# Kernel tuning notes

Hardware: AMD Instinct MI355X
Metric: run time of the kernel (lower is better)

Reference implementation:

```python
import jax, jax.numpy as jnp
import numpy as np

B, L, C, D, H = 32, 4096, 64, 512, 720
EPS = 1e-5

def _xavier(key, shape):
    fan_in, fan_out = shape
    lim = float(np.sqrt(6.0 / (fan_in + fan_out)))
    return jax.random.uniform(key, shape, minval=-lim, maxval=lim, dtype=jnp.float32)

def setup_inputs() -> dict:
    key = jax.random.key(0)
    ks = jax.random.split(key, 8)
    return {
        "x": jax.random.normal(ks[0], (B, L, C), dtype=jnp.float32),
        "alpha": jnp.full((C,), 0.5, dtype=jnp.float32),
        "rev_w": jnp.ones((C,), dtype=jnp.float32),
        "rev_b": jnp.zeros((C,), dtype=jnp.float32),
        "se_w": _xavier(ks[1], (C, D)), "se_b": jnp.zeros((D,), jnp.float32),
        "sp_w": _xavier(ks[2], (D, C)), "sp_b": jnp.zeros((C,), jnp.float32),
        "st_w": _xavier(ks[3], (L, H)), "st_b": jnp.zeros((H,), jnp.float32),
        "te_w": _xavier(ks[4], (C, D)), "te_b": jnp.zeros((D,), jnp.float32),
        "tp_w": _xavier(ks[5], (D, C)), "tp_b": jnp.zeros((C,), jnp.float32),
        "tt_w": _xavier(ks[6], (L, H)), "tt_b": jnp.zeros((H,), jnp.float32),
    }

def _path(z, ew, eb, pw, pb, tw, tb):
    # z: (B,L,C) -> embed C->D -> (identity backbone) -> proj D->C -> temporal L->H
    h = z @ ew + eb            # (B,L,D)
    h = h @ pw + pb            # (B,L,C)
    h = jnp.einsum('blc,lh->bhc', h, tw) + tb[None, :, None]  # (B,H,C)
    return h

def reference(x, alpha, rev_w, rev_b, se_w, se_b, sp_w, sp_b, st_w, st_b,
              te_w, te_b, tp_w, tp_b, tt_w, tt_b):
    # RevIN norm (stats detached, var unbiased=False)
    mean = jax.lax.stop_gradient(jnp.mean(x, axis=1, keepdims=True))          # (B,1,C)
    stdev = jax.lax.stop_gradient(jnp.sqrt(jnp.var(x, axis=1, keepdims=True) + EPS))
    xn = (x - mean) / stdev * rev_w + rev_b
    # EMA decomposition: trend[t] = a*trend[t-1] + (1-a)*x[t], trend[0]=x[0]
    a = jax.nn.sigmoid(alpha)  # (C,)
    def step(carry, xt):
        nxt = a * carry + (1.0 - a) * xt
        return nxt, nxt
    t0 = xn[:, 0]                                    # (B,C)
    _, tr = jax.lax.scan(step, t0, jnp.swapaxes(xn, 0, 1)[1:])  # (L-1,B,C)
    trend = jnp.swapaxes(jnp.concatenate([t0[None], tr], axis=0), 0, 1)  # (B,L,C)
    seasonal = xn - trend
    out = _path(seasonal, se_w, se_b, sp_w, sp_b, st_w, st_b) \
        + _path(trend,    te_w, te_b, tp_w, tp_b, tt_w, tt_b)   # (B,H,C)
    # RevIN denorm
    out = (out - rev_b) / (rev_w + EPS)
    out = out * stdev + mean
    return out
```

## Files before the change

kernel.cpp:

```cpp
#include <hip/hip_runtime.h>
#include <hip/hip_bf16.h>
#include <string.h>
#include <stdint.h>

typedef __hip_bfloat16 bf16_t;
typedef float f32x4 __attribute__((ext_vector_type(4)));
typedef short bf16x8 __attribute__((ext_vector_type(8)));

static constexpr int Bn = 32, Ln = 4096, Cn = 64, Hn = 720, HPn = 768;
static constexpr float EPSf = 1e-5f;

static constexpr size_t OSR_SLICE = (size_t)Bn * Hn * Cn;

__device__ __forceinline__ short f2bf(float f) {
  bf16_t h = __float2bfloat16(f);
  unsigned short u; memcpy(&u, &h, 2);
  return (short)u;
}

__device__ __forceinline__ float sigm(float v) { return 1.f / (1.f + expf(-v)); }

__global__ void __launch_bounds__(256) k_prep(const float* __restrict__ se_w, const float* __restrict__ sp_w,
                                              const float* __restrict__ se_b, const float* __restrict__ sp_b,
                                              const float* __restrict__ te_w, const float* __restrict__ tp_w,
                                              const float* __restrict__ te_b, const float* __restrict__ tp_b,
                                              float* __restrict__ M, float* __restrict__ cvec) {
  int p = blockIdx.y, dc = blockIdx.x, t = threadIdx.x;
  const float* ew = p ? te_w : se_w;
  const float* pw = p ? tp_w : sp_w;
  const float* eb = p ? te_b : se_b;
  const float* pb = p ? tp_b : sp_b;
  int d0 = dc * 64;
  __shared__ float ews[64][68];
  __shared__ float pws[64][68];
  __shared__ float ebs[64];
#pragma unroll
  for (int q = 0; q < 4; ++q) {
    int fi = t * 4 + q;
    int r = fi >> 4, dd = (fi * 4) & 63;
    *reinterpret_cast<f32x4*>(&ews[r][dd]) = *reinterpret_cast<const f32x4*>(&ew[r * 512 + d0 + dd]);
    int pdd = fi >> 4, c = (fi * 4) & 63;
    *reinterpret_cast<f32x4*>(&pws[pdd][c]) = *reinterpret_cast<const f32x4*>(&pw[(d0 + pdd) * 64 + c]);
  }
  if (t < 64) ebs[t] = eb[d0 + t];
  __syncthreads();
  int r0 = (t >> 4) * 4, c0 = (t & 15) * 4;
  float acc[4][4];
#pragma unroll
  for (int i = 0; i < 4; ++i)
#pragma unroll
    for (int j = 0; j < 4; ++j) acc[i][j] = 0.f;
#pragma unroll 4
  for (int g = 0; g < 16; ++g) {
    int dd = g * 4;
    f32x4 av[4], bv[4];
#pragma unroll
    for (int i = 0; i < 4; ++i) av[i] = *reinterpret_cast<const f32x4*>(&ews[r0 + i][dd]);
#pragma unroll
    for (int d = 0; d < 4; ++d) bv[d] = *reinterpret_cast<const f32x4*>(&pws[dd + d][c0]);
#pragma unroll
    for (int d = 0; d < 4; ++d)
#pragma unroll
      for (int i = 0; i < 4; ++i)
#pragma unroll
        for (int j = 0; j < 4; ++j) acc[i][j] = fmaf(av[i][d], bv[d][j], acc[i][j]);
  }
#pragma unroll
  for (int i = 0; i < 4; ++i)
#pragma unroll
    for (int j = 0; j < 4; ++j)
      atomicAdd(&M[p * 4096 + (r0 + i) * 64 + c0 + j], acc[i][j]);
  if (t < 64) {
    float s = (dc == 0) ? pb[t] : 0.f;
#pragma unroll 8
    for (int dd = 0; dd < 64; ++dd) s = fmaf(ebs[dd], pws[dd][t], s);
    atomicAdd(&cvec[p * 64 + t], s);
  }
}

__global__ void k_wprep(const float* __restrict__ st_w, const float* __restrict__ tt_w,
                        bf16_t* __restrict__ Wt, float* __restrict__ S) {
  int p = blockIdx.z;
  const float* W = p ? tt_w : st_w;
  int l0 = blockIdx.x * 64, h0 = blockIdx.y * 64;
  __shared__ float tile[64][65];
  int row = threadIdx.x >> 6, col = threadIdx.x & 63;
  int h = h0 + col;
  float partial = 0.f;
  for (int r = row; r < 64; r += 4) {
    float v = (h < Hn) ? W[(size_t)(l0 + r) * Hn + h] : 0.f;
    tile[r][col] = v;
    partial += v;
  }
  if (h < Hn) atomicAdd(&S[p * 768 + h], partial);
  __syncthreads();
  short* AF = (short*)Wt + (size_t)p * HPn * Ln;
#pragma unroll
  for (int u = 0; u < 2; ++u) {
    int uid = u * 256 + threadIdx.x;
    int ln = uid & 63, ktl = (uid >> 6) & 1, htl = uid >> 7;
    int fr = ln & 15, hi = ln >> 4;
    int ll = ktl * 32 + hi * 8;
    int hh = htl * 16 + fr;
    bf16x8 v;
#pragma unroll
    for (int e = 0; e < 8; ++e) v[e] = f2bf(tile[ll + e][hh]);
    size_t ht = (size_t)(h0 >> 4) + htl, ktg = (size_t)(l0 >> 5) + ktl;
    *reinterpret_cast<bf16x8*>(&AF[((ht * 128 + ktg) << 9) + ((size_t)ln << 3)]) = v;
  }
}

__global__ void __launch_bounds__(256) k_scanA(const float* __restrict__ x, const float* __restrict__ alpha,
                                               float* __restrict__ Psub, float* __restrict__ Pseg,
                                               float* __restrict__ Ssum, float* __restrict__ Ssq) {
  int b = blockIdx.x, q = threadIdx.y, s = blockIdx.y * 4 + q, t = threadIdx.x;
  int c4 = (t & 15) * 4, sub = t >> 4;
  float a[4], k1[4];
#pragma unroll
  for (int i = 0; i < 4; ++i) { a[i] = sigm(alpha[c4 + i]); k1[i] = 1.f - a[i]; }
  const float* xb = x + ((size_t)b * Ln + s * 64 + sub * 16) * Cn + c4;
  float pr[4] = {0.f, 0.f, 0.f, 0.f}, sm[4] = {0.f, 0.f, 0.f, 0.f}, sq[4] = {0.f, 0.f, 0.f, 0.f};
#pragma unroll
  for (int j = 0; j < 16; ++j) {
    f32x4 v = *reinterpret_cast<const f32x4*>(xb + (size_t)j * Cn);
#pragma unroll
    for (int i = 0; i < 4; ++i) {
      sm[i] += v[i];
      sq[i] = fmaf(v[i], v[i], sq[i]);
      pr[i] = fmaf(a[i], pr[i], k1[i] * v[i]);
    }
  }
  *reinterpret_cast<f32x4*>(&Psub[(((size_t)b * 64 + s) * 4 + sub) * 64 + c4]) =
      (f32x4){pr[0], pr[1], pr[2], pr[3]};
  __shared__ float lp[4][4][64], ls[4][4][64], lq[4][4][64];
#pragma unroll
  for (int i = 0; i < 4; ++i) { lp[q][sub][c4 + i] = pr[i]; ls[q][sub][c4 + i] = sm[i]; lq[q][sub][c4 + i] = sq[i]; }
  __syncthreads();
  int c = t;
  float av = sigm(alpha[c]);
  float a16 = av * av; a16 *= a16; a16 *= a16; a16 *= a16;
  float P = ((lp[q][0][c] * a16 + lp[q][1][c]) * a16 + lp[q][2][c]) * a16 + lp[q][3][c];
  int idx = (b * 64 + s) * 64 + c;
  Pseg[idx] = P;
  Ssum[idx] = ls[q][0][c] + ls[q][1][c] + ls[q][2][c] + ls[q][3][c];
  Ssq[idx]  = lq[q][0][c] + lq[q][1][c] + lq[q][2][c] + lq[q][3][c];
}

__global__ void __launch_bounds__(64) k_scanB(const float* __restrict__ x, const float* __restrict__ alpha,
                                              const float* __restrict__ rev_w, const float* __restrict__ rev_b,
                                              const float* __restrict__ Pseg, const float* __restrict__ Ssum,
                                              const float* __restrict__ Ssq,
                                              float* __restrict__ mean, float* __restrict__ rstd,
                                              float* __restrict__ stdv, float* __restrict__ CarryIn) {
  int b = blockIdx.x, c = threadIdx.x;
  float sm = 0.f, sq = 0.f;
#pragma unroll 8
  for (int s = 0; s < 64; ++s) {
    int idx = (b * 64 + s) * 64 + c;
    sm += Ssum[idx]; sq += Ssq[idx];
  }
  float mn = sm * (1.f / 4096.f);
  float var = sq * (1.f / 4096.f) - mn * mn;
  float sd = sqrtf(var + EPSf);
  float rs = 1.f / sd;
  mean[b * 64 + c] = mn; stdv[b * 64 + c] = sd; rstd[b * 64 + c] = rs;

  float w = rev_w[c], rb = rev_b[c];
  float g = rs * w, d = rb - mn * g;
  float a = sigm(alpha[c]);
  float a2 = a * a, a4 = a2 * a2, a8 = a4 * a4, a16 = a8 * a8, a32 = a16 * a16;
  float a64 = a32 * a32;
  float dk1s = d * (1.f - a64);
  float carry = fmaf(g, x[((size_t)b * Ln) * Cn + c], d);
  for (int so = 0; so < 8; ++so) {
    float pv[8];
#pragma unroll
    for (int i = 0; i < 8; ++i)
      pv[i] = Pseg[((size_t)(b * 64 + so * 8 + i)) * 64 + c];
#pragma unroll
    for (int i = 0; i < 8; ++i) {
      CarryIn[((size_t)(b * 64 + so * 8 + i)) * 64 + c] = carry;
      carry = fmaf(a64, carry, fmaf(g, pv[i], dk1s));
    }
  }
}

__global__ void __launch_bounds__(256) k_scanC(const float* __restrict__ x, const float* __restrict__ alpha,
                                               const float* __restrict__ rev_w, const float* __restrict__ rev_b,
                                               const float* __restrict__ mean, const float* __restrict__ rstd,
                                               const float* __restrict__ CarryIn, const float* __restrict__ Psub,
                                               bf16_t* __restrict__ Zt) {
  int b = blockIdx.x, ty = threadIdx.y, s = blockIdx.y * 4 + ty, t = threadIdx.x;
  int c4 = (t & 15) * 4, sub = t >> 4;
  float g[4], d[4], a[4], k1[4], a16[4], dk[4], tr[4];
#pragma unroll
  for (int i = 0; i < 4; ++i) {
    int c = c4 + i;
    float rs = rstd[b * 64 + c];
    g[i] = rs * rev_w[c]; d[i] = rev_b[c] - mean[b * 64 + c] * g[i];
    a[i] = sigm(alpha[c]); k1[i] = 1.f - a[i];
    float v = a[i] * a[i]; v *= v; v *= v; v *= v;
    a16[i] = v;
    dk[i] = d[i] * (1.f - v);
  }
  f32x4 cs = *reinterpret_cast<const f32x4*>(&CarryIn[((size_t)b * 64 + s) * 64 + c4]);
#pragma unroll
  for (int i = 0; i < 4; ++i) tr[i] = cs[i];
  for (int k = 0; k < sub; ++k) {
    f32x4 p = *reinterpret_cast<const f32x4*>(&Psub[(((size_t)b * 64 + s) * 4 + k) * 64 + c4]);
#pragma unroll
    for (int i = 0; i < 4; ++i) tr[i] = fmaf(a16[i], tr[i], fmaf(g[i], p[i], dk[i]));
  }
  const float* xb = x + ((size_t)b * Ln + s * 64 + sub * 16) * Cn + c4;
  bf16x8 vs[4][2], vt[4][2];
#pragma unroll
  for (int j = 0; j < 16; ++j) {
    f32x4 v = *reinterpret_cast<const f32x4*>(xb + (size_t)j * Cn);
#pragma unroll
    for (int i = 0; i < 4; ++i) {
      float xn = fmaf(g[i], v[i], d[i]);
      tr[i] = fmaf(a[i], tr[i], k1[i] * xn);
      vs[i][j >> 3][j & 7] = f2bf(xn - tr[i]);
      vt[i][j >> 3][j & 7] = f2bf(tr[i]);
    }
  }
  __shared__ short stage[4][8][520];
  short* BF0 = (short*)Zt;
  const size_t PATH = (size_t)Bn * Cn * Ln;
  int cq = (t & 15) >> 2;
  int u = cq * 2 + (sub >> 1);
  int hb = (sub & 1) * 2;
#pragma unroll
  for (int i = 0; i < 4; ++i) {
    int frv = (c4 & 15) + i;
    *reinterpret_cast<bf16x8*>(&stage[ty][u][(hb * 16 + frv) * 8]) = vs[i][0];
    *reinterpret_cast<bf16x8*>(&stage[ty][u][((hb + 1) * 16 + frv) * 8]) = vs[i][1];
  }
#pragma unroll
  for (int uu = 0; uu < 8; ++uu) {
    size_t nt = (size_t)b * 4 + (uu >> 1), ktg = (size_t)s * 2 + (uu & 1);
    *reinterpret_cast<bf16x8*>(BF0 + ((nt * 128 + ktg) << 9) + ((size_t)t << 3)) =
        *reinterpret_cast<const bf16x8*>(&stage[ty][uu][t * 8]);
  }
#pragma unroll
  for (int i = 0; i < 4; ++i) {
    int frv = (c4 & 15) + i;
    *reinterpret_cast<bf16x8*>(&stage[ty][u][(hb * 16 + frv) * 8]) = vt[i][0];
    *reinterpret_cast<bf16x8*>(&stage[ty][u][((hb + 1) * 16 + frv) * 8]) = vt[i][1];
  }
#pragma unroll
  for (int uu = 0; uu < 8; ++uu) {
    size_t nt = (size_t)b * 4 + (uu >> 1), ktg = (size_t)s * 2 + (uu & 1);
    *reinterpret_cast<bf16x8*>(BF0 + PATH + ((nt * 128 + ktg) << 9) + ((size_t)t << 3)) =
        *reinterpret_cast<const bf16x8*>(&stage[ty][uu][t * 8]);
  }
}

template <int KS>
__global__ void __launch_bounds__(256, 3) k_gemm(const bf16_t* __restrict__ Wt, const bf16_t* __restrict__ Zt,
                                                 float* __restrict__ Osr) {
  int per = gridDim.x >> 3;
  int swz = (blockIdx.x & 7) * per + (blockIdx.x >> 3);
  int z = swz / 96, rem = swz % 96;
  int by = rem >> 4, bx = rem & 15;
  int p = z / KS, kq = z % KS;
  const short* AF = (const short*)Wt + (size_t)p * HPn * Ln;
  const short* BF = (const short*)Zt + (size_t)p * (Bn * Cn) * Ln;
  int h0 = by * 128, n0 = bx * 128;
  int kbase = kq * (Ln / KS);
  const int NT = (Ln / KS) / 32;
  int tid = threadIdx.x, wid = tid >> 6, lane = tid & 63;
  int wr = wid >> 1, wc = wid & 1;
  int fr = lane & 15, hi = lane >> 4;
  const short* ab = AF + ((((size_t)(h0 >> 4) + wr * 4) * 128 + (kbase >> 5)) << 9) + ((size_t)lane << 3);
  const short* bb = BF + ((((size_t)(n0 >> 4) + wc * 4) * 128 + (kbase >> 5)) << 9) + ((size_t)lane << 3);

  f32x4 acc[4][4];
#pragma unroll
  for (int i = 0; i < 4; ++i)
#pragma unroll
    for (int j = 0; j < 4; ++j) acc[i][j] = (f32x4){0.f, 0.f, 0.f, 0.f};

  auto LOAD = [&](bf16x8 (&a)[4], bf16x8 (&b)[4], int kt) {
#pragma unroll
    for (int i = 0; i < 4; ++i)
      a[i] = *reinterpret_cast<const bf16x8*>(ab + (((size_t)i * 128 + kt) << 9));
#pragma unroll
    for (int j = 0; j < 4; ++j)
      b[j] = *reinterpret_cast<const bf16x8*>(bb + (((size_t)j * 128 + kt) << 9));
  };
  auto COMPUTE = [&](const bf16x8 (&a)[4], const bf16x8 (&b)[4]) {
    __builtin_amdgcn_s_setprio(1);
#pragma unroll
    for (int i = 0; i < 4; ++i)
#pragma unroll
      for (int j = 0; j < 4; ++j)
        acc[i][j] = __builtin_amdgcn_mfma_f32_16x16x32_bf16(a[i], b[j], acc[i][j], 0, 0, 0);
    __builtin_amdgcn_s_setprio(0);
  };

  bf16x8 aA[4], bA[4], aB[4], bB[4];
  LOAD(aA, bA, 0);
  for (int t = 0; t < NT; t += 2) {
    if (t + 1 < NT) LOAD(aB, bB, t + 1);
    __builtin_amdgcn_s_barrier();
    COMPUTE(aA, bA);
    if (t + 2 < NT) LOAD(aA, bA, t + 2);
    __builtin_amdgcn_s_barrier();
    if (t + 1 < NT) COMPUTE(aB, bB);
  }

#pragma unroll
  for (int i = 0; i < 4; ++i) {
#pragma unroll
    for (int j = 0; j < 4; ++j) {
#pragma unroll
      for (int r = 0; r < 4; ++r) {
        int m = wr * 64 + i * 16 + hi * 4 + r;
        int h = h0 + m;
        if (h < Hn) {
          int n = n0 + wc * 64 + j * 16 + fr;
          int bidx = n >> 6, c = n & 63;
          Osr[(((size_t)z * Bn + bidx) * Hn + h) * Cn + c] = acc[i][j][r];
        }
      }
    }
  }
}

template <int KS>
__global__ void __launch_bounds__(256) k_epi(const float* __restrict__ Osr, const float* __restrict__ M,
                                             const float* __restrict__ cvec, const float* __restrict__ S,
                                             const float* __restrict__ st_b, const float* __restrict__ tt_b,
                                             const float* __restrict__ rev_w, const float* __restrict__ rev_b,
                                             const float* __restrict__ mean, const float* __restrict__ stdv,
                                             float* __restrict__ out) {
  __shared__ float Msh[2][64][64];
  __shared__ float rowS[32][64];
  __shared__ float rowT[32][64];
  int t = threadIdx.x;
  for (int i = t; i < 2048; i += 256)
    reinterpret_cast<f32x4*>(Msh)[i] = reinterpret_cast<const f32x4*>(M)[i];
  int c = t & 63, grp = t >> 6;
  float w = rev_w[c], rb = rev_b[c];
  float cs = cvec[c], ct = cvec[64 + c];
  int base = blockIdx.x * 32;
#pragma unroll
  for (int k = 0; k < 8; ++k) {
    int rl = grp * 8 + k;
    int r = base + rl;
    int b = r / 720, h = r % 720;
    float vs = 0.f, vt = 0.f;
#pragma unroll
    for (int kq = 0; kq < KS; ++kq) {
      vs += Osr[(((size_t)kq * Bn + b) * Hn + h) * Cn + c];
      vt += Osr[(((size_t)(KS + kq) * Bn + b) * Hn + h) * Cn + c];
    }
    rowS[rl][c] = vs;
    rowT[rl][c] = vt;
  }
  __syncthreads();
  float acc[8];
  int hh[8], bb[8];
#pragma unroll
  for (int k = 0; k < 8; ++k) {
    int r = base + grp * 8 + k;
    bb[k] = r / 720; hh[k] = r % 720;
    acc[k] = cs * S[hh[k]] + ct * S[768 + hh[k]] + st_b[hh[k]] + tt_b[hh[k]];
  }
  int r0 = grp * 8;
  for (int cq = 0; cq < 16; ++cq) {
    f32x4 rs[8], rt[8];
#pragma unroll
    for (int k = 0; k < 8; ++k) rs[k] = *reinterpret_cast<const f32x4*>(&rowS[r0 + k][cq * 4]);
#pragma unroll
    for (int k = 0; k < 8; ++k) rt[k] = *reinterpret_cast<const f32x4*>(&rowT[r0 + k][cq * 4]);
#pragma unroll
    for (int i = 0; i < 4; ++i) {
      float m0 = Msh[0][cq * 4 + i][c], m1 = Msh[1][cq * 4 + i][c];
#pragma unroll
      for (int k = 0; k < 8; ++k)
        acc[k] = fmaf(rs[k][i], m0, fmaf(rt[k][i], m1, acc[k]));
    }
  }
  float winv = 1.f / (w + EPSf);
#pragma unroll
  for (int k = 0; k < 8; ++k) {
    float o = (acc[k] - rb) * winv * stdv[bb[k] * Cn + c] + mean[bb[k] * Cn + c];
    out[(size_t)(base + r0 + k) * 64 + c] = o;
  }
}

extern "C" void kernel_launch(void* const* d_in, const int* in_sizes, int n_in,
                              void* d_out, int out_size, void* d_ws, size_t ws_size,
                              hipStream_t stream) {
  const float* x     = (const float*)d_in[0];
  const float* alpha = (const float*)d_in[1];
  const float* rev_w = (const float*)d_in[2];
  const float* rev_b = (const float*)d_in[3];
  const float* se_w  = (const float*)d_in[4];
  const float* se_b  = (const float*)d_in[5];
  const float* sp_w  = (const float*)d_in[6];
  const float* sp_b  = (const float*)d_in[7];
  const float* st_w  = (const float*)d_in[8];
  const float* st_b  = (const float*)d_in[9];
  const float* te_w  = (const float*)d_in[10];
  const float* te_b  = (const float*)d_in[11];
  const float* tp_w  = (const float*)d_in[12];
  const float* tp_b  = (const float*)d_in[13];
  const float* tt_w  = (const float*)d_in[14];
  const float* tt_b  = (const float*)d_in[15];
  float* out = (float*)d_out;

  const size_t SZ_WT  = (size_t)2 * HPn * Ln * 2;
  const size_t SZ_ZT  = (size_t)2 * Bn * Cn * Ln * 2;
  const size_t SZ_SEG = (size_t)Bn * 64 * 64 * 4;
  const size_t SZ_M   = 2 * 64 * 64 * 4;
  const size_t SZ_CV  = 2 * 64 * 4;
  const size_t SZ_S   = 2 * 768 * 4;
  const size_t TAIL   = SZ_M + SZ_CV + SZ_S + 3 * (size_t)Bn * Cn * 4;

  const size_t NEED4 = SZ_WT + SZ_ZT + 8 * OSR_SLICE * 4 + TAIL;
  const int KS = (ws_size >= NEED4) ? 4 : 1;
  const size_t SZ_OSR = (size_t)(2 * KS) * OSR_SLICE * 4;

  char* ws = (char*)d_ws;
  bf16_t* Wt   = (bf16_t*)(ws);
  bf16_t* Zt   = (bf16_t*)(ws + SZ_WT);
  float*  Osr  = (float*)(ws + SZ_WT + SZ_ZT);
  float*  Psub  = Osr;
  float*  Pseg  = (float*)((char*)Psub + 4 * SZ_SEG);
  float*  Ssum  = (float*)((char*)Pseg + SZ_SEG);
  float*  Ssq   = (float*)((char*)Ssum + SZ_SEG);
  float*  Carry = (float*)((char*)Ssq + SZ_SEG);
  char* tail = ws + SZ_WT + SZ_ZT + SZ_OSR;
  float* Mbuf = (float*)tail;                 tail += SZ_M;
  float* cvec = (float*)tail;                 tail += SZ_CV;
  float* S    = (float*)tail;                 tail += SZ_S;
  float* mean = (float*)tail;                 tail += (size_t)Bn * Cn * 4;
  float* rstd = (float*)tail;                 tail += (size_t)Bn * Cn * 4;
  float* stdv = (float*)tail;

  hipMemsetAsync(Mbuf, 0, SZ_M + SZ_CV + SZ_S, stream);

  k_prep<<<dim3(8, 2), 256, 0, stream>>>(se_w, sp_w, se_b, sp_b, te_w, tp_w, te_b, tp_b, Mbuf, cvec);
  k_wprep<<<dim3(64, 12, 2), 256, 0, stream>>>(st_w, tt_w, Wt, S);
  k_scanA<<<dim3(32, 16), dim3(64, 4), 0, stream>>>(x, alpha, Psub, Pseg, Ssum, Ssq);
  k_scanB<<<32, 64, 0, stream>>>(x, alpha, rev_w, rev_b, Pseg, Ssum, Ssq, mean, rstd, stdv, Carry);
  k_scanC<<<dim3(32, 16), dim3(64, 4), 0, stream>>>(x, alpha, rev_w, rev_b, mean, rstd, Carry, Psub, Zt);
  if (KS == 4) {
    k_gemm<4><<<768, 256, 0, stream>>>(Wt, Zt, Osr);
    k_epi<4><<<720, 256, 0, stream>>>(Osr, Mbuf, cvec, S, st_b, tt_b, rev_w, rev_b, mean, stdv, out);
  } else {
    k_gemm<1><<<192, 256, 0, stream>>>(Wt, Zt, Osr);
    k_epi<1><<<720, 256, 0, stream>>>(Osr, Mbuf, cvec, S, st_b, tt_b, rev_w, rev_b, mean, stdv, out);
  }
}
```

Baseline: 107.0 us.

## Merge prep, weight-prep and scan stages into two multi-role launches without atomics

Folds k_prep, k_wprep and k_scanA into one k_pre launch, with the block index picking the role. It also folds k_scanB and the column-sum reduction into a single k_mid launch. Atomics and the memset are replaced by per-block partial sums (Spart) that are reduced deterministically afterwards. The goal is to cut launch count and per-launch overhead and to let independent work share the GPU. In exchange, the M/cvec prep now runs serially in only two blocks, which could become a long-running straggler.

New measurement: 108.0 us. Within noise of the previous version (+0.9%).

```diff
diff --git a/kernel.cpp b/kernel.cpp
--- a/kernel.cpp
+++ b/kernel.cpp
@@ -20,168 +20,202 @@
 
 __device__ __forceinline__ float sigm(float v) { return 1.f / (1.f + expf(-v)); }
 
-__global__ void __launch_bounds__(256) k_prep(const float* __restrict__ se_w, const float* __restrict__ sp_w,
-                                              const float* __restrict__ se_b, const float* __restrict__ sp_b,
-                                              const float* __restrict__ te_w, const float* __restrict__ tp_w,
-                                              const float* __restrict__ te_b, const float* __restrict__ tp_b,
-                                              float* __restrict__ M, float* __restrict__ cvec) {
-  int p = blockIdx.y, dc = blockIdx.x, t = threadIdx.x;
-  const float* ew = p ? te_w : se_w;
-  const float* pw = p ? tp_w : sp_w;
-  const float* eb = p ? te_b : se_b;
-  const float* pb = p ? tp_b : sp_b;
-  int d0 = dc * 64;
-  __shared__ float ews[64][68];
-  __shared__ float pws[64][68];
-  __shared__ float ebs[64];
-#pragma unroll
-  for (int q = 0; q < 4; ++q) {
-    int fi = t * 4 + q;
-    int r = fi >> 4, dd = (fi * 4) & 63;
-    *reinterpret_cast<f32x4*>(&ews[r][dd]) = *reinterpret_cast<const f32x4*>(&ew[r * 512 + d0 + dd]);
-    int pdd = fi >> 4, c = (fi * 4) & 63;
-    *reinterpret_cast<f32x4*>(&pws[pdd][c]) = *reinterpret_cast<const f32x4*>(&pw[(d0 + pdd) * 64 + c]);
-  }
-  if (t < 64) ebs[t] = eb[d0 + t];
-  __syncthreads();
-  int r0 = (t >> 4) * 4, c0 = (t & 15) * 4;
-  float acc[4][4];
-#pragma unroll
-  for (int i = 0; i < 4; ++i)
-#pragma unroll
-    for (int j = 0; j < 4; ++j) acc[i][j] = 0.f;
+__global__ void __launch_bounds__(256) k_pre(
+    const float* __restrict__ se_w, const float* __restrict__ sp_w,
+    const float* __restrict__ se_b, const float* __restrict__ sp_b,
+    const float* __restrict__ te_w, const float* __restrict__ tp_w,
+    const float* __restrict__ te_b, const float* __restrict__ tp_b,
+    const float* __restrict__ st_w, const float* __restrict__ tt_w,
+    const float* __restrict__ x, const float* __restrict__ alpha,
+    float* __restrict__ M, float* __restrict__ cvec, bf16_t* __restrict__ Wt,
+    float* __restrict__ Spart,
+    float* __restrict__ Psub, float* __restrict__ Pseg,
+    float* __restrict__ Ssum, float* __restrict__ Ssq) {
+  __shared__ __align__(16) char smem[35072];
+  int bid = blockIdx.x, t = threadIdx.x;
+
+  if (bid < 2) {
+    float (*ews)[68] = (float(*)[68])smem;
+    float (*pws)[68] = (float(*)[68])(smem + 17408);
+    float* ebs = (float*)(smem + 34816);
+    int p = bid;
+    const float* ew = p ? te_w : se_w;
+    const float* pw = p ? tp_w : sp_w;
+    const float* eb = p ? te_b : se_b;
+    const float* pb = p ? tp_b : sp_b;
+    int r0 = (t >> 4) * 4, c0 = (t & 15) * 4;
+    float acc[4][4];
+#pragma unroll
+    for (int i = 0; i < 4; ++i)
+#pragma unroll
+      for (int j = 0; j < 4; ++j) acc[i][j] = 0.f;
+    float cv = 0.f;
+    for (int dc = 0; dc < 8; ++dc) {
+      int d0 = dc * 64;
+#pragma unroll
+      for (int q = 0; q < 4; ++q) {
+        int fi = t * 4 + q;
+        int r = fi >> 4, dd = (fi * 4) & 63;
+        *reinterpret_cast<f32x4*>(&ews[r][dd]) = *reinterpret_cast<const f32x4*>(&ew[r * 512 + d0 + dd]);
+        *reinterpret_cast<f32x4*>(&pws[r][dd]) = *reinterpret_cast<const f32x4*>(&pw[(d0 + r) * 64 + dd]);
+      }
+      if (t < 64) ebs[t] = eb[d0 + t];
+      __syncthreads();
 #pragma unroll 4
-  for (int g = 0; g < 16; ++g) {
-    int dd = g * 4;
-    f32x4 av[4], bv[4];
-#pragma unroll
-    for (int i = 0; i < 4; ++i) av[i] = *reinterpret_cast<const f32x4*>(&ews[r0 + i][dd]);
-#pragma unroll
-    for (int d = 0; d < 4; ++d) bv[d] = *reinterpret_cast<const f32x4*>(&pws[dd + d][c0]);
-#pragma unroll
-    for (int d = 0; d < 4; ++d)
-#pragma unroll
-      for (int i = 0; i < 4; ++i)
-#pragma unroll
-        for (int j = 0; j < 4; ++j) acc[i][j] = fmaf(av[i][d], bv[d][j], acc[i][j]);
-  }
-#pragma unroll
-  for (int i = 0; i < 4; ++i)
-#pragma unroll
-    for (int j = 0; j < 4; ++j)
-      atomicAdd(&M[p * 4096 + (r0 + i) * 64 + c0 + j], acc[i][j]);
-  if (t < 64) {
-    float s = (dc == 0) ? pb[t] : 0.f;
+      for (int g = 0; g < 16; ++g) {
+        int dd = g * 4;
+        f32x4 av[4], bv[4];
+#pragma unroll
+        for (int i = 0; i < 4; ++i) av[i] = *reinterpret_cast<const f32x4*>(&ews[r0 + i][dd]);
+#pragma unroll
+        for (int d = 0; d < 4; ++d) bv[d] = *reinterpret_cast<const f32x4*>(&pws[dd + d][c0]);
+#pragma unroll
+        for (int d = 0; d < 4; ++d)
+#pragma unroll
+          for (int i = 0; i < 4; ++i)
+#pragma unroll
+            for (int j = 0; j < 4; ++j) acc[i][j] = fmaf(av[i][d], bv[d][j], acc[i][j]);
+      }
+      if (t < 64) {
 #pragma unroll 8
-    for (int dd = 0; dd < 64; ++dd) s = fmaf(ebs[dd], pws[dd][t], s);
-    atomicAdd(&cvec[p * 64 + t], s);
-  }
-}
-
-__global__ void k_wprep(const float* __restrict__ st_w, const float* __restrict__ tt_w,
-                        bf16_t* __restrict__ Wt, float* __restrict__ S) {
-  int p = blockIdx.z;
-  const float* W = p ? tt_w : st_w;
-  int l0 = blockIdx.x * 64, h0 = blockIdx.y * 64;
-  __shared__ float tile[64][65];
-  int row = threadIdx.x >> 6, col = threadIdx.x & 63;
-  int h = h0 + col;
-  float partial = 0.f;
-  for (int r = row; r < 64; r += 4) {
-    float v = (h < Hn) ? W[(size_t)(l0 + r) * Hn + h] : 0.f;
-    tile[r][col] = v;
-    partial += v;
-  }
-  if (h < Hn) atomicAdd(&S[p * 768 + h], partial);
-  __syncthreads();
-  short* AF = (short*)Wt + (size_t)p * HPn * Ln;
-#pragma unroll
-  for (int u = 0; u < 2; ++u) {
-    int uid = u * 256 + threadIdx.x;
-    int ln = uid & 63, ktl = (uid >> 6) & 1, htl = uid >> 7;
-    int fr = ln & 15, hi = ln >> 4;
-    int ll = ktl * 32 + hi * 8;
-    int hh = htl * 16 + fr;
-    bf16x8 v;
-#pragma unroll
-    for (int e = 0; e < 8; ++e) v[e] = f2bf(tile[ll + e][hh]);
-    size_t ht = (size_t)(h0 >> 4) + htl, ktg = (size_t)(l0 >> 5) + ktl;
-    *reinterpret_cast<bf16x8*>(&AF[((ht * 128 + ktg) << 9) + ((size_t)ln << 3)]) = v;
-  }
-}
-
-__global__ void __launch_bounds__(256) k_scanA(const float* __restrict__ x, const float* __restrict__ alpha,
-                                               float* __restrict__ Psub, float* __restrict__ Pseg,
-                                               float* __restrict__ Ssum, float* __restrict__ Ssq) {
-  int b = blockIdx.x, q = threadIdx.y, s = blockIdx.y * 4 + q, t = threadIdx.x;
-  int c4 = (t & 15) * 4, sub = t >> 4;
-  float a[4], k1[4];
-#pragma unroll
-  for (int i = 0; i < 4; ++i) { a[i] = sigm(alpha[c4 + i]); k1[i] = 1.f - a[i]; }
-  const float* xb = x + ((size_t)b * Ln + s * 64 + sub * 16) * Cn + c4;
-  float pr[4] = {0.f, 0.f, 0.f, 0.f}, sm[4] = {0.f, 0.f, 0.f, 0.f}, sq[4] = {0.f, 0.f, 0.f, 0.f};
-#pragma unroll
-  for (int j = 0; j < 16; ++j) {
-    f32x4 v = *reinterpret_cast<const f32x4*>(xb + (size_t)j * Cn);
+        for (int dd = 0; dd < 64; ++dd) cv = fmaf(ebs[dd], pws[dd][t], cv);
+      }
+      __syncthreads();
+    }
+#pragma unroll
+    for (int i = 0; i < 4; ++i)
+#pragma unroll
+      for (int j = 0; j < 4; ++j)
+        M[p * 4096 + (r0 + i) * 64 + c0 + j] = acc[i][j];
+    if (t < 64) cvec[p * 64 + t] = cv + pb[t];
+
+  } else if (bid < 514) {
+    float (*lp)[64] = (float(*)[64])smem;
+    float (*ls)[64] = (float(*)[64])(smem + 4096);
+    float (*lq)[64] = (float(*)[64])(smem + 8192);
+    int idx = bid - 2;
+    int b = idx >> 4, sg = idx & 15;
+    int ty = t >> 6, tx = t & 63;
+    int s = sg * 4 + ty;
+    int c4 = (tx & 15) * 4, sub = tx >> 4;
+    float a[4], k1[4];
+#pragma unroll
+    for (int i = 0; i < 4; ++i) { a[i] = sigm(alpha[c4 + i]); k1[i] = 1.f - a[i]; }
+    const float* xb = x + ((size_t)b * Ln + s * 64 + sub * 16) * Cn + c4;
+    float pr[4] = {0.f, 0.f, 0.f, 0.f}, sm[4] = {0.f, 0.f, 0.f, 0.f}, sq[4] = {0.f, 0.f, 0.f, 0.f};
+#pragma unroll
+    for (int j = 0; j < 16; ++j) {
+      f32x4 v = *reinterpret_cast<const f32x4*>(xb + (size_t)j * Cn);
+#pragma unroll
+      for (int i = 0; i < 4; ++i) {
+        sm[i] += v[i];
+        sq[i] = fmaf(v[i], v[i], sq[i]);
+        pr[i] = fmaf(a[i], pr[i], k1[i] * v[i]);
+      }
+    }
+    *reinterpret_cast<f32x4*>(&Psub[(((size_t)b * 64 + s) * 4 + sub) * 64 + c4]) =
+        (f32x4){pr[0], pr[1], pr[2], pr[3]};
 #pragma unroll
     for (int i = 0; i < 4; ++i) {
-      sm[i] += v[i];
-      sq[i] = fmaf(v[i], v[i], sq[i]);
-      pr[i] = fmaf(a[i], pr[i], k1[i] * v[i]);
-    }
-  }
-  *reinterpret_cast<f32x4*>(&Psub[(((size_t)b * 64 + s) * 4 + sub) * 64 + c4]) =
-      (f32x4){pr[0], pr[1], pr[2], pr[3]};
-  __shared__ float lp[4][4][64], ls[4][4][64], lq[4][4][64];
-#pragma unroll
-  for (int i = 0; i < 4; ++i) { lp[q][sub][c4 + i] = pr[i]; ls[q][sub][c4 + i] = sm[i]; lq[q][sub][c4 + i] = sq[i]; }
-  __syncthreads();
-  int c = t;
-  float av = sigm(alpha[c]);
-  float a16 = av * av; a16 *= a16; a16 *= a16; a16 *= a16;
-  float P = ((lp[q][0][c] * a16 + lp[q][1][c]) * a16 + lp[q][2][c]) * a16 + lp[q][3][c];
-  int idx = (b * 64 + s) * 64 + c;
-  Pseg[idx] = P;
-  Ssum[idx] = ls[q][0][c] + ls[q][1][c] + ls[q][2][c] + ls[q][3][c];
-  Ssq[idx]  = lq[q][0][c] + lq[q][1][c] + lq[q][2][c] + lq[q][3][c];
-}
-
-__global__ void __launch_bounds__(64) k_scanB(const float* __restrict__ x, const float* __restrict__ alpha,
-                                              const float* __restrict__ rev_w, const float* __restrict__ rev_b,
-                                              const float* __restrict__ Pseg, const float* __restrict__ Ssum,
-                                              const float* __restrict__ Ssq,
-                                              float* __restrict__ mean, float* __restrict__ rstd,
-                                              float* __restrict__ stdv, float* __restrict__ CarryIn) {
-  int b = blockIdx.x, c = threadIdx.x;
-  float sm = 0.f, sq = 0.f;
+      lp[ty * 4 + sub][c4 + i] = pr[i];
+      ls[ty * 4 + sub][c4 + i] = sm[i];
+      lq[ty * 4 + sub][c4 + i] = sq[i];
+    }
+    __syncthreads();
+    int c = tx;
+    float av = sigm(alpha[c]);
+    float a16 = av * av; a16 *= a16; a16 *= a16; a16 *= a16;
+    float P = ((lp[ty * 4 + 0][c] * a16 + lp[ty * 4 + 1][c]) * a16 + lp[ty * 4 + 2][c]) * a16 + lp[ty * 4 + 3][c];
+    int oidx = (b * 64 + s) * 64 + c;
+    Pseg[oidx] = P;
+    Ssum[oidx] = ls[ty * 4 + 0][c] + ls[ty * 4 + 1][c] + ls[ty * 4 + 2][c] + ls[ty * 4 + 3][c];
+    Ssq[oidx]  = lq[ty * 4 + 0][c] + lq[ty * 4 + 1][c] + lq[ty * 4 + 2][c] + lq[ty * 4 + 3][c];
+
+  } else {
+    float (*tile)[65] = (float(*)[65])smem;
+    float (*colsum)[64] = (float(*)[64])(smem + 16640);
+    int idx = bid - 514;
+    int p = idx / 768, rem = idx % 768;
+    int lc = rem & 63, hc = rem >> 6;
+    const float* W = p ? tt_w : st_w;
+    int l0 = lc * 64, h0 = hc * 64;
+    int row = t >> 6, col = t & 63;
+    int h = h0 + col;
+    float partial = 0.f;
+    for (int r = row; r < 64; r += 4) {
+      float v = (h < Hn) ? W[(size_t)(l0 + r) * Hn + h] : 0.f;
+      tile[r][col] = v;
+      partial += v;
+    }
+    colsum[row][col] = partial;
+    __syncthreads();
+    if (row == 0)
+      Spart[((size_t)p * 64 + lc) * 768 + h] = colsum[0][col] + colsum[1][col] + colsum[2][col] + colsum[3][col];
+    short* AF = (short*)Wt + (size_t)p * HPn * Ln;
+#pragma unroll
+    for (int u = 0; u < 2; ++u) {
+      int uid = u * 256 + t;
+      int ln = uid & 63, ktl = (uid >> 6) & 1, htl = uid >> 7;
+      int fr = ln & 15, hi = ln >> 4;
+      int ll = ktl * 32 + hi * 8;
+      int hh = htl * 16 + fr;
+      bf16x8 v;
+#pragma unroll
+      for (int e = 0; e < 8; ++e) v[e] = f2bf(tile[ll + e][hh]);
+      size_t ht = (size_t)(h0 >> 4) + htl, ktg = (size_t)(l0 >> 5) + ktl;
+      *reinterpret_cast<bf16x8*>(&AF[((ht * 128 + ktg) << 9) + ((size_t)ln << 3)]) = v;
+    }
+  }
+}
+
+__global__ void __launch_bounds__(256) k_mid(
+    const float* __restrict__ x, const float* __restrict__ alpha,
+    const float* __restrict__ rev_w, const float* __restrict__ rev_b,
+    const float* __restrict__ Pseg, const float* __restrict__ Ssum, const float* __restrict__ Ssq,
+    const float* __restrict__ Spart,
+    float* __restrict__ mean, float* __restrict__ rstd, float* __restrict__ stdv,
+    float* __restrict__ CarryIn, float* __restrict__ S) {
+  int bid = blockIdx.x, t = threadIdx.x;
+  if (bid < 8) {
+    int b = bid * 4 + (t >> 6), c = t & 63;
+    float sm = 0.f, sq = 0.f;
 #pragma unroll 8
-  for (int s = 0; s < 64; ++s) {
-    int idx = (b * 64 + s) * 64 + c;
-    sm += Ssum[idx]; sq += Ssq[idx];
-  }
-  float mn = sm * (1.f / 4096.f);
-  float var = sq * (1.f / 4096.f) - mn * mn;
-  float sd = sqrtf(var + EPSf);
-  float rs = 1.f / sd;
-  mean[b * 64 + c] = mn; stdv[b * 64 + c] = sd; rstd[b * 64 + c] = rs;
-
-  float w = rev_w[c], rb = rev_b[c];
-  float g = rs * w, d = rb - mn * g;
-  float a = sigm(alpha[c]);
-  float a2 = a * a, a4 = a2 * a2, a8 = a4 * a4, a16 = a8 * a8, a32 = a16 * a16;
-  float a64 = a32 * a32;
-  float dk1s = d * (1.f - a64);
-  float carry = fmaf(g, x[((size_t)b * Ln) * Cn + c], d);
-  for (int so = 0; so < 8; ++so) {
-    float pv[8];
-#pragma unroll
-    for (int i = 0; i < 8; ++i)
-      pv[i] = Pseg[((size_t)(b * 64 + so * 8 + i)) * 64 + c];
-#pragma unroll
-    for (int i = 0; i < 8; ++i) {
-      CarryIn[((size_t)(b * 64 + so * 8 + i)) * 64 + c] = carry;
-      carry = fmaf(a64, carry, fmaf(g, pv[i], dk1s));
-    }
+    for (int s = 0; s < 64; ++s) {
+      int idx = (b * 64 + s) * 64 + c;
+      sm += Ssum[idx]; sq += Ssq[idx];
+    }
+    float mn = sm * (1.f / 4096.f);
+    float var = sq * (1.f / 4096.f) - mn * mn;
+    float sd = sqrtf(var + EPSf);
+    float rs = 1.f / sd;
+    mean[b * 64 + c] = mn; stdv[b * 64 + c] = sd; rstd[b * 64 + c] = rs;
+
+    float w = rev_w[c], rb = rev_b[c];
+    float g = rs * w, d = rb - mn * g;
+    float a = sigm(alpha[c]);
+    float a2 = a * a, a4 = a2 * a2, a8 = a4 * a4, a16 = a8 * a8, a32 = a16 * a16;
+    float a64 = a32 * a32;
+    float dk1s = d * (1.f - a64);
+    float carry = fmaf(g, x[((size_t)b * Ln) * Cn + c], d);
+    for (int so = 0; so < 8; ++so) {
+      float pv[8];
+#pragma unroll
+      for (int i = 0; i < 8; ++i)
+        pv[i] = Pseg[((size_t)(b * 64 + so * 8 + i)) * 64 + c];
+#pragma unroll
+      for (int i = 0; i < 8; ++i) {
+        CarryIn[((size_t)(b * 64 + so * 8 + i)) * 64 + c] = carry;
+        carry = fmaf(a64, carry, fmaf(g, pv[i], dk1s));
+      }
+    }
+  } else {
+    int idx = (bid - 8) * 256 + t;
+    int p = idx / 768, h = idx % 768;
+    float s = 0.f;
+#pragma unroll 8
+    for (int lc = 0; lc < 64; ++lc)
+      s += Spart[((size_t)p * 64 + lc) * 768 + h];
+    S[p * 768 + h] = s;
   }
 }
 
@@ -418,7 +452,8 @@
   const size_t SZ_M   = 2 * 64 * 64 * 4;
   const size_t SZ_CV  = 2 * 64 * 4;
   const size_t SZ_S   = 2 * 768 * 4;
-  const size_t TAIL   = SZ_M + SZ_CV + SZ_S + 3 * (size_t)Bn * Cn * 4;
+  const size_t SZ_SP  = (size_t)2 * 64 * 768 * 4;
+  const size_t TAIL   = SZ_M + SZ_CV + SZ_S + SZ_SP + 3 * (size_t)Bn * Cn * 4;
 
   const size_t NEED4 = SZ_WT + SZ_ZT + 8 * OSR_SLICE * 4 + TAIL;
   const int KS = (ws_size >= NEED4) ? 4 : 1;
@@ -437,16 +472,16 @@
   float* Mbuf = (float*)tail;                 tail += SZ_M;
   float* cvec = (float*)tail;                 tail += SZ_CV;
   float* S    = (float*)tail;                 tail += SZ_S;
+  float* Spart = (float*)tail;                tail += SZ_SP;
   float* mean = (float*)tail;                 tail += (size_t)Bn * Cn * 4;
   float* rstd = (float*)tail;                 tail += (size_t)Bn * Cn * 4;
   float* stdv = (float*)tail;
 
-  hipMemsetAsync(Mbuf, 0, SZ_M + SZ_CV + SZ_S, stream);
-
-  k_prep<<<dim3(8, 2), 256, 0, stream>>>(se_w, sp_w, se_b, sp_b, te_w, tp_w, te_b, tp_b, Mbuf, cvec);
-  k_wprep<<<dim3(64, 12, 2), 256, 0, stream>>>(st_w, tt_w, Wt, S);
-  k_scanA<<<dim3(32, 16), dim3(64, 4), 0, stream>>>(x, alpha, Psub, Pseg, Ssum, Ssq);
-  k_scanB<<<32, 64, 0, stream>>>(x, alpha, rev_w, rev_b, Pseg, Ssum, Ssq, mean, rstd, stdv, Carry);
+  k_pre<<<2050, 256, 0, stream>>>(se_w, sp_w, se_b, sp_b, te_w, tp_w, te_b, tp_b,
+                                  st_w, tt_w, x, alpha, Mbuf, cvec, Wt, Spart,
+                                  Psub, Pseg, Ssum, Ssq);
+  k_mid<<<14, 256, 0, stream>>>(x, alpha, rev_w, rev_b, Pseg, Ssum, Ssq, Spart,
+                                mean, rstd, stdv, Carry, S);
   k_scanC<<<dim3(32, 16), dim3(64, 4), 0, stream>>>(x, alpha, rev_w, rev_b, mean, rstd, Carry, Psub, Zt);
   if (KS == 4) {
     k_gemm<4><<<768, 256, 0, stream>>>(Wt, Zt, Osr);
```
